# Performance work log

Hardware: AMD Instinct MI355X
Metric: run time of the kernel (lower is better)

Reference implementation:

```python
import jax, jax.numpy as jnp
import numpy as np

EPS = 1e-5
SLOPE = 0.2
K = 20


def _knn(x, k):
    # x: [B, C, N] -> indices of k nearest neighbors [B, N, k] (self included, largest neg sq dist)
    sq = jnp.sum(x * x, axis=1)  # [B, N]
    pd = 2.0 * jnp.einsum('bcn,bcm->bnm', x, x) - sq[:, :, None] - sq[:, None, :]
    return jax.lax.top_k(pd, k)[1]


def _graph_feature(x, k):
    # x: [B, C, N] -> edge features [B, 2C, N, k]
    B, C, N = x.shape
    idx = _knn(x, k)                                   # [B, N, k]
    xt = jnp.transpose(x, (0, 2, 1))                   # [B, N, C]
    nb = xt[jnp.arange(B)[:, None, None], idx]         # [B, N, k, C] gather neighbors
    ctr = jnp.broadcast_to(xt[:, :, None, :], (B, N, k, C))
    f = jnp.concatenate([nb - ctr, ctr], axis=-1)      # [B, N, k, 2C]
    return jnp.transpose(f, (0, 3, 1, 2))              # [B, 2C, N, k]


def _bn_act(y, g, b, m, v):
    # eval-mode batchnorm over channel axis 1 + leaky relu(0.2); y rank 3 or 4
    shp = (1, -1) + (1,) * (y.ndim - 2)
    scale = (g / jnp.sqrt(v + EPS)).reshape(shp)
    shift = (b - m * g / jnp.sqrt(v + EPS)).reshape(shp)
    y = y * scale + shift
    return jnp.where(y >= 0, y, SLOPE * y)


def _edge_block(x, k, W, g, b, m, v):
    f = _graph_feature(x, k)                           # [B, 2C, N, k]
    y = jnp.einsum('oc,bcnk->bonk', W, f)              # 1x1 conv2d, no bias
    y = _bn_act(y, g, b, m, v)
    return jnp.max(y, axis=-1)                         # max over k neighbors -> [B, O, N]


def setup_inputs() -> dict:
    key = jax.random.key(0)
    ks = jax.random.split(key, 8)
    B, N = 16, 2048
    d = {'object_pc': jax.random.normal(ks[0], (B, N, 3), dtype=jnp.float32)}
    dims = [(64, 6), (64, 128), (128, 128), (256, 256), (256, 512)]
    for i, (o, c) in enumerate(dims, start=1):
        d[f'W{i}'] = jax.random.normal(ks[i], (o, c), dtype=jnp.float32) / np.sqrt(c)
        d[f'g{i}'] = jnp.ones((o,), jnp.float32)
        d[f'b{i}'] = jnp.zeros((o,), jnp.float32)
        d[f'm{i}'] = jnp.zeros((o,), jnp.float32)
        d[f'v{i}'] = jnp.ones((o,), jnp.float32)
    return d


def reference(object_pc, W1, g1, b1, m1, v1, W2, g2, b2, m2, v2,
              W3, g3, b3, m3, v3, W4, g4, b4, m4, v4, W5, g5, b5, m5, v5):
    x = jnp.transpose(object_pc, (0, 2, 1))            # [B, 3, N]
    x1 = _edge_block(x, K, W1, g1, b1, m1, v1)         # [B, 64, N]
    x2 = _edge_block(x1, K, W2, g2, b2, m2, v2)        # [B, 64, N]
    x3 = _edge_block(x2, K, W3, g3, b3, m3, v3)        # [B, 128, N]
    x4 = _edge_block(x3, K, W4, g4, b4, m4, v4)        # [B, 256, N]
    cat = jnp.concatenate([x1, x2, x3, x4], axis=1)    # [B, 512, N]
    y = jnp.einsum('oc,bcn->bon', W5, cat)             # 1x1 conv1d
    y = _bn_act(y, g5, b5, m5, v5)
    return jnp.max(y, axis=-1)                         # global max pool -> [B, emb_dim]
```

## Files before the change

kernel.cpp:

```cpp
#include <hip/hip_runtime.h>

#define NPTS 2048
#define KNN_K 20
#define BATCH 16

constexpr float EPSV   = 1e-5f;
constexpr float SLOPEV = 0.2f;

__device__ __forceinline__ float dot4(float4 a, float4 b, float acc) {
  acc = fmaf(a.x, b.x, acc);
  acc = fmaf(a.y, b.y, acc);
  acc = fmaf(a.z, b.z, acc);
  acc = fmaf(a.w, b.w, acc);
  return acc;
}

#define INSERT20(VAL, IDXV)                                              \
  if ((VAL) > topd[KNN_K - 1]) {                                         \
    float d_ = (VAL); int i_ = (IDXV);                                   \
    _Pragma("unroll")                                                    \
    for (int j_ = 0; j_ < KNN_K; ++j_) {                                 \
      bool sw_ = d_ > topd[j_];                                          \
      float td_ = sw_ ? d_ : topd[j_]; float dd_ = sw_ ? topd[j_] : d_;  \
      int   ti_ = sw_ ? i_ : topi[j_]; int  di_ = sw_ ? topi[j_] : i_;   \
      topd[j_] = td_; d_ = dd_; topi[j_] = ti_; i_ = di_;                \
    }                                                                    \
  }

__global__ void pad_kernel(const float* __restrict__ pc, float* __restrict__ X0P) {
  int i = blockIdx.x * 256 + threadIdx.x;
  float4 v;
  v.x = pc[i * 3 + 0]; v.y = pc[i * 3 + 1]; v.z = pc[i * 3 + 2]; v.w = 0.f;
  ((float4*)X0P)[i] = v;
}

template<int C>
__global__ void sq_kernel(const float* __restrict__ XT, float* __restrict__ SQ) {
  int i = blockIdx.x * 256 + threadIdx.x;
  const float4* r4 = (const float4*)(XT + (long)i * C);
  float s = 0.f;
  #pragma unroll
  for (int c = 0; c < C / 4; ++c) { float4 v = r4[c]; s = dot4(v, v, s); }
  SQ[i] = s;
}

template<int C>
__global__ __launch_bounds__(256, 2) void dist_kernel(const float* __restrict__ X,
                                                      const float* __restrict__ SQc,
                                                      float* __restrict__ D) {
  constexpr int KC = (C % 8 == 0) ? 8 : C;
  __shared__ float As[KC][132];
  __shared__ float Bs[KC][132];
  __shared__ float Ts[16][132];
  int lin = blockIdx.x;
  int bb = lin / 136;
  int tid = lin - bb * 136;
  int tn = 0, rem = tid;
  while (rem >= 16 - tn) { rem -= 16 - tn; ++tn; }
  int tm = tn + rem;
  int t = threadIdx.x;
  int tx = t & 15, ty = t >> 4;
  long base = (long)bb * NPTS;
  const float* Xb = X + base * C;
  int n0 = tn * 128, m0 = tm * 128;

  float acc[8][8];
  #pragma unroll
  for (int i = 0; i < 8; ++i)
    #pragma unroll
    for (int j = 0; j < 8; ++j) acc[i][j] = 0.f;

  for (int k0 = 0; k0 < C; k0 += KC) {
    for (int e = t; e < 32 * KC; e += 256) {
      int row = e / (KC / 4), c4 = e % (KC / 4);
      float4 v = *(const float4*)(Xb + (long)(n0 + row) * C + k0 + c4 * 4);
      As[c4 * 4 + 0][row] = v.x; As[c4 * 4 + 1][row] = v.y;
      As[c4 * 4 + 2][row] = v.z; As[c4 * 4 + 3][row] = v.w;
    }
    for (int e = t; e < 32 * KC; e += 256) {
      int row = e / (KC / 4), c4 = e % (KC / 4);
      float4 v = *(const float4*)(Xb + (long)(m0 + row) * C + k0 + c4 * 4);
      Bs[c4 * 4 + 0][row] = v.x; Bs[c4 * 4 + 1][row] = v.y;
      Bs[c4 * 4 + 2][row] = v.z; Bs[c4 * 4 + 3][row] = v.w;
    }
    __syncthreads();
    #pragma unroll
    for (int k = 0; k < KC; ++k) {
      float4 a0 = *(const float4*)&As[k][ty * 8];
      float4 a1 = *(const float4*)&As[k][ty * 8 + 4];
      float4 b0 = *(const float4*)&Bs[k][tx * 8];
      float4 b1 = *(const float4*)&Bs[k][tx * 8 + 4];
      float av[8] = {a0.x, a0.y, a0.z, a0.w, a1.x, a1.y, a1.z, a1.w};
      float bv[8] = {b0.x, b0.y, b0.z, b0.w, b1.x, b1.y, b1.z, b1.w};
      #pragma unroll
      for (int i = 0; i < 8; ++i)
        #pragma unroll
        for (int j = 0; j < 8; ++j)
          acc[i][j] = fmaf(av[i], bv[j], acc[i][j]);
    }
    __syncthreads();
  }

  float sqn[8], sqm[8];
  #pragma unroll
  for (int i = 0; i < 8; ++i) sqn[i] = SQc[base + n0 + ty * 8 + i];
  #pragma unroll
  for (int j = 0; j < 8; ++j) sqm[j] = SQc[base + m0 + tx * 8 + j];

  #pragma unroll
  for (int i = 0; i < 8; ++i)
    #pragma unroll
    for (int j = 0; j < 8; ++j)
      acc[i][j] = fmaf(2.f, acc[i][j], -sqn[i]) - sqm[j];

  #pragma unroll
  for (int i = 0; i < 8; ++i) {
    float* drow = D + (base + n0 + ty * 8 + i) * NPTS + m0 + tx * 8;
    float4 w0, w1;
    w0.x = acc[i][0]; w0.y = acc[i][1]; w0.z = acc[i][2]; w0.w = acc[i][3];
    w1.x = acc[i][4]; w1.y = acc[i][5]; w1.z = acc[i][6]; w1.w = acc[i][7];
    *(float4*)drow = w0;
    *(float4*)(drow + 4) = w1;
  }

  if (tn != tm) {
    for (int s = 0; s < 8; ++s) {
      if ((tx >> 1) == s) {
        #pragma unroll
        for (int j = 0; j < 8; ++j)
          #pragma unroll
          for (int i = 0; i < 8; ++i)
            Ts[(tx & 1) * 8 + j][ty * 8 + i] = acc[i][j];
      }
      __syncthreads();
      for (int e = t; e < 16 * 32; e += 256) {
        int rr = e >> 5, c4 = e & 31;
        *(float4*)(D + (base + m0 + s * 16 + rr) * NPTS + n0 + c4 * 4) =
            *(const float4*)&Ts[rr][c4 * 4];
      }
      __syncthreads();
    }
  }
}

__global__ __launch_bounds__(256, 2) void select_kernel(const float* __restrict__ D,
                                                        int* __restrict__ IDXc) {
  __shared__ float ld[256][KNN_K];
  __shared__ int   li[256][KNN_K];
  int t = threadIdx.x;
  int rloc = t >> 3, q = t & 7;
  long row = (long)blockIdx.x * 32 + rloc;
  const float4* dr = (const float4*)(D + row * NPTS + q * 256);

  float topd[KNN_K]; int topi[KNN_K];
  #pragma unroll
  for (int j = 0; j < KNN_K; ++j) { topd[j] = -3e38f; topi[j] = 0; }

  int mb = q * 256;
  #pragma unroll 1
  for (int j4 = 0; j4 < 64; j4 += 4) {
    float4 v0 = dr[j4 + 0];
    float4 v1 = dr[j4 + 1];
    float4 v2 = dr[j4 + 2];
    float4 v3 = dr[j4 + 3];
    int m = mb + j4 * 4;
    INSERT20(v0.x, m + 0);
    INSERT20(v0.y, m + 1);
    INSERT20(v0.z, m + 2);
    INSERT20(v0.w, m + 3);
    INSERT20(v1.x, m + 4);
    INSERT20(v1.y, m + 5);
    INSERT20(v1.z, m + 6);
    INSERT20(v1.w, m + 7);
    INSERT20(v2.x, m + 8);
    INSERT20(v2.y, m + 9);
    INSERT20(v2.z, m + 10);
    INSERT20(v2.w, m + 11);
    INSERT20(v3.x, m + 12);
    INSERT20(v3.y, m + 13);
    INSERT20(v3.z, m + 14);
    INSERT20(v3.w, m + 15);
  }

  #pragma unroll
  for (int j = 0; j < KNN_K; ++j) { ld[t][j] = topd[j]; li[t][j] = topi[j]; }
  __syncthreads();

  if (q == 0) {
    int* dst = IDXc + row * KNN_K;
    int ia[8];
    #pragma unroll
    for (int l = 0; l < 8; ++l) ia[l] = 0;
    for (int j = 0; j < KNN_K; ++j) {
      float best = ld[t][ia[0]]; int bl = 0;
      #pragma unroll
      for (int l = 1; l < 8; ++l) {
        float v = ld[t + l][ia[l]];
        if (v > best) { best = v; bl = l; }
      }
      dst[j] = li[t + bl][ia[bl]];
      #pragma unroll
      for (int l = 0; l < 8; ++l) ia[l] += (l == bl) ? 1 : 0;
    }
  }
}

template<int O, int C>
__global__ __launch_bounds__(256, 2) void conv_small(const float* __restrict__ XTin,
                                                     const int* __restrict__ IDX,
                                                     const float* __restrict__ W,
                                                     const float* __restrict__ gg,
                                                     const float* __restrict__ bbias,
                                                     const float* __restrict__ mmean,
                                                     const float* __restrict__ vvar,
                                                     float* __restrict__ XTout) {
  constexpr int G   = 256 / O;
  constexpr int KPG = KNN_K / G;
  __shared__ float cols[KNN_K + 1][C];

  int bid = blockIdx.x;
  int b = bid >> 11, n = bid & 2047;
  int t = threadIdx.x;
  long rowbase = ((long)b << 11);
  const int* idxp = IDX + (long)bid * KNN_K;

  for (int e = t; e < (KNN_K + 1) * C; e += 256) {
    int col = e / C, c = e - col * C;
    int j = (col == 0) ? n : idxp[col - 1];
    cols[col][c] = XTin[(rowbase + j) * C + c];
  }
  __syncthreads();

  int o = t / G, kg = t - o * G;
  const float* wrow = W + o * (2 * C);

  float acc[KPG];
  #pragma unroll
  for (int q = 0; q < KPG; ++q) acc[q] = 0.f;
  float s1 = 0.f, u2 = 0.f;

  #pragma unroll
  for (int c = 0; c < C; ++c) {
    float w1 = wrow[c];
    float w2 = wrow[C + c];
    float xn = cols[0][c];
    s1 = fmaf(w1, xn, s1);
    u2 = fmaf(w2, xn, u2);
    #pragma unroll
    for (int q = 0; q < KPG; ++q) {
      int k = kg * KPG + q;
      acc[q] = fmaf(w1, cols[1 + k][c], acc[q]);
    }
  }

  float sc = gg[o] / sqrtf(vvar[o] + EPSV);
  float sh = bbias[o] - mmean[o] * sc;
  float vmax = -3e38f;
  #pragma unroll
  for (int q = 0; q < KPG; ++q) {
    float z = acc[q] - s1 + u2;
    float y = fmaf(sc, z, sh);
    y = (y >= 0.f) ? y : SLOPEV * y;
    vmax = fmaxf(vmax, y);
  }
  #pragma unroll
  for (int off = 1; off < G; off <<= 1)
    vmax = fmaxf(vmax, __shfl_xor(vmax, off, 64));
  if (kg == 0) XTout[(rowbase + n) * O + o] = vmax;
}

template<int O, int C>
__global__ __launch_bounds__(256, 2) void ad_kernel(const float* __restrict__ X,
                                                    const float* __restrict__ W,
                                                    float* __restrict__ A,
                                                    float* __restrict__ BASE) {
  static_assert(C % 4 == 0 && 256 % O == 0, "ad shape");
  constexpr int G  = 256 / O;
  constexpr int NP = 16 / G;
  constexpr int C4 = C / 4;
  __shared__ float xs[16][C];

  int blk = blockIdx.x;
  long m0 = (long)blk * 16;
  int t = threadIdx.x;

  for (int e = t; e < 16 * C4; e += 256) {
    int pt = e / C4, c4 = e - pt * C4;
    *(float4*)&xs[pt][c4 * 4] = *(const float4*)(X + (m0 + pt) * C + c4 * 4);
  }
  __syncthreads();

  int o = t % O, pg = t / O;
  const float* wrow = W + o * (2 * C);

  float accA[NP], accD[NP];
  #pragma unroll
  for (int q = 0; q < NP; ++q) { accA[q] = 0.f; accD[q] = 0.f; }

  for (int c4 = 0; c4 < C4; ++c4) {
    float4 w1 = *(const float4*)(wrow + c4 * 4);
    float4 w2 = *(const float4*)(wrow + C + c4 * 4);
    #pragma unroll
    for (int q = 0; q < NP; ++q) {
      float4 xv = *(const float4*)&xs[pg * NP + q][c4 * 4];
      accA[q] = dot4(w1, xv, accA[q]);
      accD[q] = dot4(w2, xv, accD[q]);
    }
  }

  #pragma unroll
  for (int q = 0; q < NP; ++q) {
    long m = m0 + pg * NP + q;
    A[m * O + o]    = accA[q];
    BASE[m * O + o] = accD[q] - accA[q];
  }
}

template<int O>
__global__ __launch_bounds__(256, 4) void gather_kernel(const float* __restrict__ A,
                                                        const int* __restrict__ IDX,
                                                        const float* __restrict__ gg,
                                                        const float* __restrict__ bbias,
                                                        const float* __restrict__ mmean,
                                                        const float* __restrict__ vvar,
                                                        float* __restrict__ XTio) {
  constexpr int PPB = 256 / O;
  int t = threadIdx.x;
  int o = t % O, pp = t / O;
  long p = (long)blockIdx.x * PPB + pp;
  int b = (int)(p >> 11);
  long rowbase = ((long)b << 11);
  const int* idxp = IDX + p * KNN_K;

  float base = XTio[p * O + o];
  float sc = gg[o] / sqrtf(vvar[o] + EPSV);
  float sh = bbias[o] - mmean[o] * sc;

  float vmax = -3e38f;
  #pragma unroll
  for (int k = 0; k < KNN_K; ++k) {
    int nb = idxp[k];
    float a = A[(rowbase + nb) * O + o];
    float y = fmaf(sc, a + base, sh);
    y = (y >= 0.f) ? y : SLOPEV * y;
    vmax = fmaxf(vmax, y);
  }
  XTio[p * O + o] = vmax;
}

__global__ __launch_bounds__(256, 2) void final_kernel(const float* __restrict__ X1,
                                                       const float* __restrict__ X2,
                                                       const float* __restrict__ X3,
                                                       const float* __restrict__ X4,
                                                       const float* __restrict__ W5,
                                                       const float* __restrict__ g5,
                                                       const float* __restrict__ b5,
                                                       const float* __restrict__ m5,
                                                       const float* __restrict__ v5,
                                                       float* __restrict__ RED) {
  __shared__ float tile[16][512];
  int bid = blockIdx.x;
  int b = bid >> 7, chunk = bid & 127;
  int n0 = chunk * 16;
  int t = threadIdx.x;

  for (int e = t; e < 16 * 128; e += 256) {
    int nn = e >> 7, c4 = e & 127;
    int c = c4 * 4;
    long row = ((long)b << 11) + n0 + nn;
    float4 v;
    if      (c < 64)  v = *(const float4*)(X1 + row * 64  + c);
    else if (c < 128) v = *(const float4*)(X2 + row * 64  + (c - 64));
    else if (c < 256) v = *(const float4*)(X3 + row * 128 + (c - 128));
    else              v = *(const float4*)(X4 + row * 256 + (c - 256));
    *(float4*)&tile[nn][c] = v;
  }
  __syncthreads();

  int o = t;
  const float* wrow = W5 + o * 512;
  float acc[16];
  #pragma unroll
  for (int q = 0; q < 16; ++q) acc[q] = 0.f;
  for (int c4 = 0; c4 < 128; ++c4) {
    float4 w = *(const float4*)(wrow + c4 * 4);
    #pragma unroll
    for (int q = 0; q < 16; ++q) {
      float4 xv = *(const float4*)&tile[q][c4 * 4];
      acc[q] = dot4(w, xv, acc[q]);
    }
  }
  float sc = g5[o] / sqrtf(v5[o] + EPSV);
  float sh = b5[o] - m5[o] * sc;
  float vmax = -3e38f;
  #pragma unroll
  for (int q = 0; q < 16; ++q) {
    float y = fmaf(sc, acc[q], sh);
    y = (y >= 0.f) ? y : SLOPEV * y;
    vmax = fmaxf(vmax, y);
  }
  RED[((long)b * 256 + o) * 128 + chunk] = vmax;
}

__global__ void reduce_kernel(const float* __restrict__ RED, float* __restrict__ out) {
  int i = blockIdx.x * 256 + threadIdx.x;
  const float* r = RED + (long)i * 128;
  float v = r[0];
  for (int j = 1; j < 128; ++j) v = fmaxf(v, r[j]);
  out[i] = v;
}

extern "C" void kernel_launch(void* const* d_in, const int* in_sizes, int n_in,
                              void* d_out, int out_size, void* d_ws, size_t ws_size,
                              hipStream_t stream) {
  (void)in_sizes; (void)n_in; (void)out_size; (void)ws_size;
  const float* pc = (const float*)d_in[0];
  const float* W1 = (const float*)d_in[1];
  const float* g1 = (const float*)d_in[2];
  const float* b1 = (const float*)d_in[3];
  const float* m1 = (const float*)d_in[4];
  const float* v1 = (const float*)d_in[5];
  const float* W2 = (const float*)d_in[6];
  const float* g2 = (const float*)d_in[7];
  const float* b2 = (const float*)d_in[8];
  const float* m2 = (const float*)d_in[9];
  const float* v2 = (const float*)d_in[10];
  const float* W3 = (const float*)d_in[11];
  const float* g3 = (const float*)d_in[12];
  const float* b3 = (const float*)d_in[13];
  const float* m3 = (const float*)d_in[14];
  const float* v3 = (const float*)d_in[15];
  const float* W4 = (const float*)d_in[16];
  const float* g4 = (const float*)d_in[17];
  const float* b4 = (const float*)d_in[18];
  const float* m4 = (const float*)d_in[19];
  const float* v4 = (const float*)d_in[20];
  const float* W5 = (const float*)d_in[21];
  const float* g5 = (const float*)d_in[22];
  const float* b5 = (const float*)d_in[23];
  const float* m5 = (const float*)d_in[24];
  const float* v5 = (const float*)d_in[25];
  float* out = (float*)d_out;

  float* XT1 = (float*)d_ws;
  float* XT2 = XT1 + 2097152;
  float* XT3 = XT2 + 2097152;
  float* XT4 = XT3 + 4194304;
  float* AD  = XT4 + 8388608;
  float* D   = XT4;
  float* SQ  = AD  + 8388608;
  float* RED = SQ  + 32768;
  int*   IDX = (int*)(RED + 524288);
  float* X0P = (float*)(IDX + 655360);

  const int BN = BATCH * NPTS;
  const long CHB = 4L * NPTS;
  const int DG = 4 * 136;

  pad_kernel<<<BN / 256, 256, 0, stream>>>(pc, X0P);
  sq_kernel<4><<<BN / 256, 256, 0, stream>>>(X0P, SQ);
  for (int ch = 0; ch < 4; ++ch) {
    dist_kernel<4><<<DG, 256, 0, stream>>>(X0P + ch * CHB * 4, SQ + ch * CHB, D);
    select_kernel<<<256, 256, 0, stream>>>(D, IDX + ch * CHB * KNN_K);
  }
  conv_small<64, 3><<<BN, 256, 0, stream>>>(pc, IDX, W1, g1, b1, m1, v1, XT1);

  sq_kernel<64><<<BN / 256, 256, 0, stream>>>(XT1, SQ);
  for (int ch = 0; ch < 4; ++ch) {
    dist_kernel<64><<<DG, 256, 0, stream>>>(XT1 + ch * CHB * 64, SQ + ch * CHB, D);
    select_kernel<<<256, 256, 0, stream>>>(D, IDX + ch * CHB * KNN_K);
  }
  ad_kernel<64, 64><<<BN / 16, 256, 0, stream>>>(XT1, W2, AD, XT2);
  gather_kernel<64><<<BN / 4, 256, 0, stream>>>(AD, IDX, g2, b2, m2, v2, XT2);

  sq_kernel<64><<<BN / 256, 256, 0, stream>>>(XT2, SQ);
  for (int ch = 0; ch < 4; ++ch) {
    dist_kernel<64><<<DG, 256, 0, stream>>>(XT2 + ch * CHB * 64, SQ + ch * CHB, D);
    select_kernel<<<256, 256, 0, stream>>>(D, IDX + ch * CHB * KNN_K);
  }
  ad_kernel<128, 64><<<BN / 16, 256, 0, stream>>>(XT2, W3, AD, XT3);
  gather_kernel<128><<<BN / 2, 256, 0, stream>>>(AD, IDX, g3, b3, m3, v3, XT3);

  sq_kernel<128><<<BN / 256, 256, 0, stream>>>(XT3, SQ);
  for (int ch = 0; ch < 4; ++ch) {
    dist_kernel<128><<<DG, 256, 0, stream>>>(XT3 + ch * CHB * 128, SQ + ch * CHB, D);
    select_kernel<<<256, 256, 0, stream>>>(D, IDX + ch * CHB * KNN_K);
  }
  ad_kernel<256, 128><<<BN / 16, 256, 0, stream>>>(XT3, W4, AD, XT4);
  gather_kernel<256><<<BN, 256, 0, stream>>>(AD, IDX, g4, b4, m4, v4, XT4);

  final_kernel<<<BATCH * 128, 256, 0, stream>>>(XT1, XT2, XT3, XT4, W5, g5, b5, m5, v5, RED);
  reduce_kernel<<<BATCH, 256, 0, stream>>>(RED, out);
}
```

Before: 2.501 ms.

## Register-tile final 1x1 conv with weight slabs staged in LDS

The final 512-to-256 conv kernel switches from one output channel per thread (each thread streaming its own weight row from global memory) to a 4x4 register tile of channels by points. Weight slabs are staged cooperatively into shared memory, and results are max-reduced across lanes with shuffles. This is meant to cut redundant, uncoalesced global weight traffic and raise arithmetic intensity per shared-memory load. In exchange it adds two barriers per k-step. The padded row stride of 17 floats makes the float4 accesses into the weight slab unaligned, which may be slow or unsafe.

```diff
diff --git a/kernel.cpp b/kernel.cpp
--- a/kernel.cpp
+++ b/kernel.cpp
@@ -358,7 +358,8 @@
                                                        const float* __restrict__ m5,
                                                        const float* __restrict__ v5,
                                                        float* __restrict__ RED) {
-  __shared__ float tile[16][512];
+  __shared__ float tile[16][516];
+  __shared__ float wslab[256][17];
   int bid = blockIdx.x;
   int b = bid >> 7, chunk = bid & 127;
   int n0 = chunk * 16;
@@ -373,33 +374,71 @@
     else if (c < 128) v = *(const float4*)(X2 + row * 64  + (c - 64));
     else if (c < 256) v = *(const float4*)(X3 + row * 128 + (c - 128));
     else              v = *(const float4*)(X4 + row * 256 + (c - 256));
-    *(float4*)&tile[nn][c] = v;
+    *(float4*)&tile[nn][c4 * 4] = v;
   }
   __syncthreads();
 
-  int o = t;
-  const float* wrow = W5 + o * 512;
-  float acc[16];
-  #pragma unroll
-  for (int q = 0; q < 16; ++q) acc[q] = 0.f;
-  for (int c4 = 0; c4 < 128; ++c4) {
-    float4 w = *(const float4*)(wrow + c4 * 4);
-    #pragma unroll
-    for (int q = 0; q < 16; ++q) {
-      float4 xv = *(const float4*)&tile[q][c4 * 4];
-      acc[q] = dot4(w, xv, acc[q]);
-    }
-  }
-  float sc = g5[o] / sqrtf(v5[o] + EPSV);
-  float sh = b5[o] - m5[o] * sc;
-  float vmax = -3e38f;
-  #pragma unroll
-  for (int q = 0; q < 16; ++q) {
-    float y = fmaf(sc, acc[q], sh);
-    y = (y >= 0.f) ? y : SLOPEV * y;
-    vmax = fmaxf(vmax, y);
-  }
-  RED[((long)b * 256 + o) * 128 + chunk] = vmax;
+  int og = t >> 2, pg = t & 3;
+  float acc[4][4];
+  #pragma unroll
+  for (int i = 0; i < 4; ++i)
+    #pragma unroll
+    for (int j = 0; j < 4; ++j) acc[i][j] = 0.f;
+
+  for (int k0 = 0; k0 < 128; k0 += 4) {
+    #pragma unroll
+    for (int l = 0; l < 4; ++l) {
+      int e = t + l * 256;
+      int o = e >> 2, part = e & 3;
+      *(float4*)&wslab[o][part * 4] = *(const float4*)(W5 + o * 512 + k0 * 4 + part * 4);
+    }
+    __syncthreads();
+    #pragma unroll
+    for (int cc = 0; cc < 4; ++cc) {
+      float4 w0 = *(const float4*)&wslab[og * 4 + 0][cc * 4];
+      float4 w1 = *(const float4*)&wslab[og * 4 + 1][cc * 4];
+      float4 w2 = *(const float4*)&wslab[og * 4 + 2][cc * 4];
+      float4 w3 = *(const float4*)&wslab[og * 4 + 3][cc * 4];
+      float4 x0 = *(const float4*)&tile[pg * 4 + 0][(k0 + cc) * 4];
+      float4 x1 = *(const float4*)&tile[pg * 4 + 1][(k0 + cc) * 4];
+      float4 x2 = *(const float4*)&tile[pg * 4 + 2][(k0 + cc) * 4];
+      float4 x3 = *(const float4*)&tile[pg * 4 + 3][(k0 + cc) * 4];
+      acc[0][0] = dot4(w0, x0, acc[0][0]);
+      acc[0][1] = dot4(w1, x0, acc[0][1]);
+      acc[0][2] = dot4(w2, x0, acc[0][2]);
+      acc[0][3] = dot4(w3, x0, acc[0][3]);
+      acc[1][0] = dot4(w0, x1, acc[1][0]);
+      acc[1][1] = dot4(w1, x1, acc[1][1]);
+      acc[1][2] = dot4(w2, x1, acc[1][2]);
+      acc[1][3] = dot4(w3, x1, acc[1][3]);
+      acc[2][0] = dot4(w0, x2, acc[2][0]);
+      acc[2][1] = dot4(w1, x2, acc[2][1]);
+      acc[2][2] = dot4(w2, x2, acc[2][2]);
+      acc[2][3] = dot4(w3, x2, acc[2][3]);
+      acc[3][0] = dot4(w0, x3, acc[3][0]);
+      acc[3][1] = dot4(w1, x3, acc[3][1]);
+      acc[3][2] = dot4(w2, x3, acc[3][2]);
+      acc[3][3] = dot4(w3, x3, acc[3][3]);
+    }
+    __syncthreads();
+  }
+
+  #pragma unroll
+  for (int j = 0; j < 4; ++j) {
+    int o = og * 4 + j;
+    float sc = g5[o] / sqrtf(v5[o] + EPSV);
+    float sh = b5[o] - m5[o] * sc;
+    float vm = -3e38f;
+    #pragma unroll
+    for (int i = 0; i < 4; ++i) {
+      float y = fmaf(sc, acc[i][j], sh);
+      y = (y >= 0.f) ? y : SLOPEV * y;
+      vm = fmaxf(vm, y);
+    }
+    vm = fmaxf(vm, __shfl_xor(vm, 1, 64));
+    vm = fmaxf(vm, __shfl_xor(vm, 2, 64));
+    if (pg == 0) RED[((long)b * 256 + o) * 128 + chunk] = vm;
+  }
 }
 
 __global__ void reduce_kernel(const float* __restrict__ RED, float* __restrict__ out) {
```

Result: faster. 2.419 ms (-3.3%).
